# Performance work log

Hardware: AMD Instinct MI355X
Metric: run time of the kernel (lower is better)

The kernel has to match this reference:

```python
import jax, jax.numpy as jnp
import numpy as np

P = 5; G = 60; E = 256; H = 8
NPD = G // P; NP = NPD ** 3          # 1728 patch tokens
LE = 4; LD = 2; NC = 40; B = 4
MASK_RATIO = 0.75
NUM_MASK = int(MASK_RATIO * NP)      # 1296 masked, 432 visible


def setup_inputs() -> dict:
    key = jax.random.key(0)
    ki = iter(jax.random.split(key, 64))
    def n(shape, s=0.02):
        return jax.random.normal(next(ki), shape, jnp.float32) * s
    d = {
        "x": jax.random.normal(next(ki), (B, 1, G, G, G), jnp.float32),
        "noise": jax.random.uniform(next(ki), (B, NP), jnp.float32),
        "patch_w": n((E, 1, P, P, P), 0.05),
        "patch_b": jnp.zeros((E,), jnp.float32),
        "pos_embed": n((1, NP, E)),
        "dec_pos_embed": n((1, NP, E)),
        "mask_token": n((1, 1, E)),
        "pred_w": n((P ** 3, E)),
        "pred_b": jnp.zeros((P ** 3,), jnp.float32),
        "cls_w": n((NC, E)),
        "cls_b": jnp.zeros((NC,), jnp.float32),
    }
    for pre, L in (("enc", LE), ("dec", LD)):
        d[pre + "_qkv_w"] = n((L, 3 * E, E)); d[pre + "_qkv_b"] = jnp.zeros((L, 3 * E), jnp.float32)
        d[pre + "_out_w"] = n((L, E, E));     d[pre + "_out_b"] = jnp.zeros((L, E), jnp.float32)
        d[pre + "_ln1_w"] = jnp.ones((L, E), jnp.float32); d[pre + "_ln1_b"] = jnp.zeros((L, E), jnp.float32)
        d[pre + "_ln2_w"] = jnp.ones((L, E), jnp.float32); d[pre + "_ln2_b"] = jnp.zeros((L, E), jnp.float32)
        d[pre + "_ffn1_w"] = n((L, 4 * E, E)); d[pre + "_ffn1_b"] = jnp.zeros((L, 4 * E), jnp.float32)
        d[pre + "_ffn2_w"] = n((L, E, 4 * E)); d[pre + "_ffn2_b"] = jnp.zeros((L, E), jnp.float32)
    return d


def _ln(x, w, b):
    m = x.mean(-1, keepdims=True)
    v = ((x - m) ** 2).mean(-1, keepdims=True)
    return (x - m) / jnp.sqrt(v + 1e-5) * w + b


def _layer(x, qkv_w, qkv_b, out_w, out_b, l1w, l1b, l2w, l2b, f1w, f1b, f2w, f2b):
    # post-norm TransformerEncoderLayer with exact-erf GELU (dropout=0 at eval)
    Bx, S, Ex = x.shape
    dh = Ex // H
    qkv = x @ qkv_w.T + qkv_b                      # [B,S,3E]
    q, k, v = jnp.split(qkv, 3, axis=-1)
    q = q.reshape(Bx, S, H, dh); k = k.reshape(Bx, S, H, dh); v = v.reshape(Bx, S, H, dh)
    scores = jnp.einsum('bqhd,bkhd->bhqk', q, k) / np.float32(np.sqrt(dh))
    attn = jax.nn.softmax(scores, axis=-1)
    o = jnp.einsum('bhqk,bkhd->bqhd', attn, v).reshape(Bx, S, Ex)
    x = _ln(x + o @ out_w.T + out_b, l1w, l1b)
    f = jax.nn.gelu(x @ f1w.T + f1b, approximate=False) @ f2w.T + f2b
    return _ln(x + f, l2w, l2b)


def _stack(x, params, L):
    for i in range(L):
        x = _layer(x, *(a[i] for a in params))
    return x


def _forward(x, noise, patch_w, patch_b, pos_embed, dec_pos_embed, mask_token,
             enc_qkv_w, enc_qkv_b, enc_out_w, enc_out_b, enc_ln1_w, enc_ln1_b, enc_ln2_w, enc_ln2_b,
             enc_ffn1_w, enc_ffn1_b, enc_ffn2_w, enc_ffn2_b,
             dec_qkv_w, dec_qkv_b, dec_out_w, dec_out_b, dec_ln1_w, dec_ln1_b, dec_ln2_w, dec_ln2_b,
             dec_ffn1_w, dec_ffn1_b, dec_ffn2_w, dec_ffn2_b,
             pred_w, pred_b, cls_w, cls_b):
    Bx = x.shape[0]
    # patchify: [B,1,G,G,G] -> [B, NP, P^3]
    xg = x.reshape(Bx, 1, NPD, P, NPD, P, NPD, P)
    xg = xg.transpose(0, 2, 4, 6, 1, 3, 5, 7).reshape(Bx, NP, P ** 3)
    # Conv3d with stride == kernel == patch embedding over flattened patches
    tokens = xg @ patch_w.reshape(E, P ** 3).T + patch_b + pos_embed   # [B,NP,E]
    # random masking
    ids_shuffle = jnp.argsort(noise, axis=1)
    ids_mask = ids_shuffle[:, :NUM_MASK]
    ids_keep = ids_shuffle[:, NUM_MASK:]                                # [B, 432]
    mask = jnp.zeros((Bx, NP), x.dtype).at[jnp.arange(Bx)[:, None], ids_mask].set(1.0)
    x_vis = jnp.take_along_axis(tokens, ids_keep[:, :, None], axis=1)   # [B,432,E]
    enc = _stack(x_vis,
                 (enc_qkv_w, enc_qkv_b, enc_out_w, enc_out_b, enc_ln1_w, enc_ln1_b,
                  enc_ln2_w, enc_ln2_b, enc_ffn1_w, enc_ffn1_b, enc_ffn2_w, enc_ffn2_b), LE)
    cls_logits = enc.mean(axis=1) @ cls_w.T + cls_b
    # scatter encoded tokens back into full mask-token buffer (vectorized over batch)
    x_dec = jnp.broadcast_to(mask_token, (Bx, NP, E))
    x_dec = jax.vmap(lambda base, ids, e: base.at[ids].set(e))(x_dec, ids_keep, enc)
    dec = _stack(x_dec + dec_pos_embed,
                 (dec_qkv_w, dec_qkv_b, dec_out_w, dec_out_b, dec_ln1_w, dec_ln1_b,
                  dec_ln2_w, dec_ln2_b, dec_ffn1_w, dec_ffn1_b, dec_ffn2_w, dec_ffn2_b), LD)
    pred = dec @ pred_w.T + pred_b                                      # [B,NP,P^3]
    return pred, xg, mask, cls_logits


def reference(x, noise, patch_w, patch_b, pos_embed, dec_pos_embed, mask_token,
              enc_qkv_w, enc_qkv_b, enc_out_w, enc_out_b, enc_ln1_w, enc_ln1_b, enc_ln2_w, enc_ln2_b,
              enc_ffn1_w, enc_ffn1_b, enc_ffn2_w, enc_ffn2_b,
              dec_qkv_w, dec_qkv_b, dec_out_w, dec_out_b, dec_ln1_w, dec_ln1_b, dec_ln2_w, dec_ln2_b,
              dec_ffn1_w, dec_ffn1_b, dec_ffn2_w, dec_ffn2_b,
              pred_w, pred_b, cls_w, cls_b):
    return _forward(x, noise, patch_w, patch_b, pos_embed, dec_pos_embed, mask_token,
                    enc_qkv_w, enc_qkv_b, enc_out_w, enc_out_b, enc_ln1_w, enc_ln1_b, enc_ln2_w, enc_ln2_b,
                    enc_ffn1_w, enc_ffn1_b, enc_ffn2_w, enc_ffn2_b,
                    dec_qkv_w, dec_qkv_b, dec_out_w, dec_out_b, dec_ln1_w, dec_ln1_b, dec_ln2_w, dec_ln2_b,
                    dec_ffn1_w, dec_ffn1_b, dec_ffn2_w, dec_ffn2_b,
                    pred_w, pred_b, cls_w, cls_b)
```

## Files before the change

kernel.cpp:

```cpp
#include <hip/hip_runtime.h>
#include <hip/hip_bf16.h>
#include <math.h>

#define E 256
#define Hh 8
#define DH 32
#define NP 1728
#define PP3 125
#define Bb 4
#define NUM_MASKC 1296
#define NKEEP 432
#define LE 4
#define LD 2
#define NC 40

typedef __attribute__((ext_vector_type(4))) float f32x4;
typedef __attribute__((ext_vector_type(8))) short bf16x8;
typedef __attribute__((ext_vector_type(4))) short s16x4;

#define QSCALE 0.25505654708402214f

__device__ inline short f2b(float f) {
    __hip_bfloat16 h = __float2bfloat16(f);
    return *reinterpret_cast<short*>(&h);
}
__device__ inline float b2f(short s) {
    union { unsigned u; float f; } v; v.u = ((unsigned)(unsigned short)s) << 16;
    return v.f;
}
__device__ inline unsigned cvt_pk(float lo, float hi) {
    unsigned r;
    asm("v_cvt_pk_bf16_f32 %0, %1, %2" : "=v"(r) : "v"(lo), "v"(hi));
    return r;
}
__device__ inline void gl_lds16(const void* g, void* l) {
    __builtin_amdgcn_global_load_lds(
        (const __attribute__((address_space(1))) void*)g,
        (__attribute__((address_space(3))) void*)l, 16, 0, 0);
}

struct W2B { const float* src; short* dst; int n; int npad; };
struct W2BTab { W2B e[25]; };
__global__ void k_w2b(W2BTab tab) {
    W2B w = tab.e[blockIdx.y];
    int i = (blockIdx.x*256 + threadIdx.x) * 8;
    if (i + 8 <= w.n) {
        float4 a = *(const float4*)(w.src + i);
        float4 b = *(const float4*)(w.src + i + 4);
        short t[8] = {f2b(a.x),f2b(a.y),f2b(a.z),f2b(a.w),
                      f2b(b.x),f2b(b.y),f2b(b.z),f2b(b.w)};
        *(bf16x8*)(w.dst + i) = *(const bf16x8*)t;
    } else if (i < w.npad) {
        *(bf16x8*)(w.dst + i) = (bf16x8)0;
    }
}

__global__ void k_rank(const float* __restrict__ noise, int* __restrict__ shuf,
                       int* __restrict__ keep_pos, float* __restrict__ out_mask)
{
    __shared__ float ns[NP];
    int b = blockIdx.x / 7, it = blockIdx.x % 7;
    const float* nr = noise + (size_t)b*NP;
    int tid = threadIdx.x;
    for (int j = tid; j < NP; j += 256) ns[j] = nr[j];
    __syncthreads();
    int i = it*256 + tid;
    if (i < NP) {
        float ni = ns[i];
        int rank = 0;
        for (int j = 0; j < NP; ++j) {
            float nj = ns[j];
            rank += (nj < ni) || (nj == ni && j < i);
        }
        shuf[b*NP + rank] = i;
        keep_pos[b*NP + i] = (rank >= NUM_MASKC) ? (rank - NUM_MASKC) : -1;
        out_mask[b*NP + i] = (rank < NUM_MASKC) ? 1.0f : 0.0f;
    }
}

__global__ void k_xg(const float* __restrict__ x, float* __restrict__ out_xg)
{
    int bn = blockIdx.x;
    int b = bn / NP, n = bn % NP;
    int a0 = n / 144, r = n % 144, b0 = r / 12, c0 = r % 12;
    int t = threadIdx.x;
    if (t < PP3) {
        int pa = t / 25, rem = t % 25, pbq = rem / 5, pc = rem % 5;
        out_xg[(size_t)bn*PP3 + t] =
            x[(size_t)b*216000 + (size_t)(a0*5+pa)*3600 + (b0*5+pbq)*60 + (c0*5+pc)];
    }
}

__global__ void k_patch_vis(const float* __restrict__ x, const float* __restrict__ pw,
                            const float* __restrict__ pb, const float* __restrict__ pos,
                            const int* __restrict__ shuf, short* __restrict__ visb)
{
    int row = blockIdx.x;
    int b = row / NKEEP, s = row % NKEEP;
    int n = shuf[b*NP + NUM_MASKC + s];
    int a0 = n / 144, r = n % 144, b0 = r / 12, c0 = r % 12;
    __shared__ float patch[PP3];
    int t = threadIdx.x;
    if (t < PP3) {
        int pa = t / 25, rem = t % 25, pbq = rem / 5, pc = rem % 5;
        patch[t] = x[(size_t)b*216000 + (size_t)(a0*5+pa)*3600 + (b0*5+pbq)*60 + (c0*5+pc)];
    }
    __syncthreads();
    float acc = pb[t] + pos[(size_t)n*E + t];
    const float* w = pw + (size_t)t*PP3;
    for (int k = 0; k < PP3; ++k) acc += patch[k] * w[k];
    visb[(size_t)row*E + t] = f2b(acc);
}

__global__ __launch_bounds__(256) void
k_mgemm(const short* __restrict__ A, const short* __restrict__ W,
        const float* __restrict__ bias, float* __restrict__ Cf,
        short* __restrict__ Cb, int M, int N, int K, int act,
        short* __restrict__ qkvb, short* __restrict__ vTb, int S)
{
    __shared__ short As[64][64];
    __shared__ short Ws[64][64];
    int tid = threadIdx.x;
    int lane = tid & 63, wave = tid >> 6;
    int rb = blockIdx.y * 64, cb = blockIdx.x * 64;
    int wr = (wave >> 1) * 32, wc = (wave & 1) * 32;
    int fr = lane & 15, fq = lane >> 4;
    f32x4 acc[2][2];
    #pragma unroll
    for (int m = 0; m < 2; ++m)
        #pragma unroll
        for (int n = 0; n < 2; ++n) acc[m][n] = (f32x4)0.f;
    int rl = lane >> 3, cl = lane & 7;
    int r0 = 16 * wave;
    for (int kk0 = 0; kk0 < K; kk0 += 64) {
        #pragma unroll
        for (int j = 0; j < 2; ++j) {
            int r = r0 + 8*j + rl;
            int cs = cl ^ (r & 7);
            gl_lds16(A + (size_t)(rb + r)*K + kk0 + cs*8, &As[r0 + 8*j][0]);
            gl_lds16(W + (size_t)(cb + r)*K + kk0 + cs*8, &Ws[r0 + 8*j][0]);
        }
        __syncthreads();
        #pragma unroll
        for (int t = 0; t < 2; ++t) {
            int rA0 = wr + fr, rA1 = wr + 16 + fr;
            int rB0 = wc + fr, rB1 = wc + 16 + fr;
            bf16x8 a0 = *(const bf16x8*)&As[rA0][(((4*t + fq) ^ (rA0 & 7)) << 3)];
            bf16x8 a1 = *(const bf16x8*)&As[rA1][(((4*t + fq) ^ (rA1 & 7)) << 3)];
            bf16x8 b0 = *(const bf16x8*)&Ws[rB0][(((4*t + fq) ^ (rB0 & 7)) << 3)];
            bf16x8 b1 = *(const bf16x8*)&Ws[rB1][(((4*t + fq) ^ (rB1 & 7)) << 3)];
            acc[0][0] = __builtin_amdgcn_mfma_f32_16x16x32_bf16(a0, b0, acc[0][0], 0, 0, 0);
            acc[0][1] = __builtin_amdgcn_mfma_f32_16x16x32_bf16(a0, b1, acc[0][1], 0, 0, 0);
            acc[1][0] = __builtin_amdgcn_mfma_f32_16x16x32_bf16(a1, b0, acc[1][0], 0, 0, 0);
            acc[1][1] = __builtin_amdgcn_mfma_f32_16x16x32_bf16(a1, b1, acc[1][1], 0, 0, 0);
        }
        __syncthreads();
    }
    #pragma unroll
    for (int m = 0; m < 2; ++m) {
        #pragma unroll
        for (int n = 0; n < 2; ++n) {
            int col = cb + wc + n*16 + fr;
            if (col >= N) continue;
            float bv = bias[col];
            #pragma unroll
            for (int r = 0; r < 4; ++r) {
                int row = rb + wr + m*16 + fq*4 + r;
                if (row >= M) continue;
                float v = acc[m][n][r] + bv;
                if (act == 1) v = 0.5f * v * (1.f + erff(v * 0.70710678118654752f));
                if (qkvb) {
                    if (col < 512) {
                        if (col < 256) v *= QSCALE;
                        qkvb[(size_t)row*768 + col] = f2b(v);
                    } else {
                        int b = row / S, s = row - b*S;
                        int hd = col - 512;
                        vTb[((size_t)(b*Hh + (hd >> 5))*DH + (hd & 31))*S + s] = f2b(v);
                    }
                } else if (Cb) {
                    Cb[(size_t)row*N + col] = f2b(v);
                } else {
                    Cf[(size_t)row*N + col] = v;
                }
            }
        }
    }
}

__global__ __launch_bounds__(128) void
k_fattn(const short* __restrict__ qkvb, const short* __restrict__ vTb,
        short* __restrict__ o, int S)
{
    __shared__ short Ks[2][64][40];
    __shared__ short Vt[2][32][72];
    int nqt = (S + 31) >> 5;
    int bi = blockIdx.x;
    int qt = bi % nqt, bh = bi / nqt;
    int h = bh & 7, b = bh >> 3;
    int q0 = qt << 5;
    int tid = threadIdx.x;
    int lane = tid & 63, wave = tid >> 6;
    int fr = lane & 15, fq = lane >> 4;
    bf16x8 qfrag = (bf16x8)0;
    int qg = q0 + wave*16 + fr;
    if (qg < S)
        qfrag = *(const bf16x8*)(qkvb + (size_t)(b*S+qg)*768 + h*DH + 8*fq);
    f32x4 acc0 = (f32x4)0.f, acc1 = (f32x4)0.f;
    float lpart = 0.f;
    int krow = tid >> 1, kh = (tid & 1) * 16;
    int vrow = tid >> 2, vk4 = (tid & 3) * 16;
    const short* kbase = qkvb + (size_t)(b*S)*768 + 256 + h*DH + (size_t)krow*768 + kh;
    const short* vTh = vTb + (size_t)bh*DH*S + (size_t)vrow*S + vk4;
    int src1 = fr + ((fq & 1) << 5);
    int src2 = src1 + 16;
    bool sel = (fq >> 1) != 0;
    int nt = (S + 63) >> 6;
    bool tail = (S & 63) != 0;
    bf16x8 kr0, kr1, vr0, vr1;
    auto LOADF = [&](int t) {
        const short* src = kbase + (size_t)(t << 6)*768;
        kr0 = *(const bf16x8*)src;
        kr1 = *(const bf16x8*)(src + 8);
        const short* vs = vTh + (t << 6);
        vr0 = *(const bf16x8*)vs;
        vr1 = *(const bf16x8*)(vs + 8);
    };
    auto LOADT = [&](int t) {
        int kg = (t << 6) + krow;
        if (kg < S) {
            const short* src = kbase + (size_t)(t << 6)*768;
            kr0 = *(const bf16x8*)src;
            kr1 = *(const bf16x8*)(src + 8);
        } else { kr0 = (bf16x8)0; kr1 = (bf16x8)0; }
        if ((t << 6) + vk4 < S) {
            const short* vs = vTh + (t << 6);
            vr0 = *(const bf16x8*)vs;
            vr1 = *(const bf16x8*)(vs + 8);
        } else { vr0 = (bf16x8)0; vr1 = (bf16x8)0; }
    };
    auto WRITE = [&](int p) {
        *(bf16x8*)&Ks[p][krow][kh]      = kr0;
        *(bf16x8*)&Ks[p][krow][kh + 8]  = kr1;
        *(bf16x8*)&Vt[p][vrow][vk4]     = vr0;
        *(bf16x8*)&Vt[p][vrow][vk4 + 8] = vr1;
    };
    LOADF(0); WRITE(0);
    __syncthreads();
    for (int t = 0; t < nt; ++t) {
        int p = t & 1;
        bool masked = tail && (t == nt - 1);
        if (t + 1 < nt) {
            if (tail && (t + 1 == nt - 1)) LOADT(t + 1); else LOADF(t + 1);
        }
        f32x4 st[4];
        #pragma unroll
        for (int kt = 0; kt < 4; ++kt) {
            bf16x8 kf = *(const bf16x8*)&Ks[p][kt*16 + fr][8*fq];
            st[kt] = __builtin_amdgcn_mfma_f32_16x16x32_bf16(kf, qfrag, (f32x4)0.f, 0, 0, 0);
        }
        if (masked) {
            int kt0 = t << 6;
            #pragma unroll
            for (int kt = 0; kt < 4; ++kt)
                #pragma unroll
                for (int r = 0; r < 4; ++r)
                    if (kt0 + kt*16 + 4*fq + r >= S) st[kt][r] = -1e30f;
        }
        float tsum = 0.f;
        unsigned pk[4][2];
        #pragma unroll
        for (int kt = 0; kt < 4; ++kt) {
            float p0 = exp2f(st[kt][0]), p1 = exp2f(st[kt][1]);
            float p2 = exp2f(st[kt][2]), p3 = exp2f(st[kt][3]);
            tsum += (p0 + p1) + (p2 + p3);
            pk[kt][0] = cvt_pk(p0, p1);
            pk[kt][1] = cvt_pk(p2, p3);
        }
        lpart += tsum;
        #pragma unroll
        for (int t2 = 0; t2 < 2; ++t2) {
            unsigned a0 = __shfl(pk[2*t2][0], src1),   a1 = __shfl(pk[2*t2][1], src1);
            unsigned a2 = __shfl(pk[2*t2][0], src2),   a3 = __shfl(pk[2*t2][1], src2);
            unsigned b0 = __shfl(pk[2*t2+1][0], src1), b1 = __shfl(pk[2*t2+1][1], src1);
            unsigned b2 = __shfl(pk[2*t2+1][0], src2), b3 = __shfl(pk[2*t2+1][1], src2);
            union { unsigned u[4]; bf16x8 v; } B2;
            B2.u[0] = sel ? b0 : a0;
            B2.u[1] = sel ? b1 : a1;
            B2.u[2] = sel ? b2 : a2;
            B2.u[3] = sel ? b3 : a3;
            bf16x8 v0 = *(const bf16x8*)&Vt[p][fr][t2*32 + 8*fq];
            bf16x8 v1 = *(const bf16x8*)&Vt[p][16 + fr][t2*32 + 8*fq];
            acc0 = __builtin_amdgcn_mfma_f32_16x16x32_bf16(v0, B2.v, acc0, 0, 0, 0);
            acc1 = __builtin_amdgcn_mfma_f32_16x16x32_bf16(v1, B2.v, acc1, 0, 0, 0);
        }
        if (t + 1 < nt) WRITE(p ^ 1);
        __syncthreads();
    }
    float lsum = lpart;
    lsum += __shfl_xor(lsum, 16);
    lsum += __shfl_xor(lsum, 32);
    if (qg < S) {
        float inv = 1.f / lsum;
        short* op = o + (size_t)(b*S + qg)*E + h*DH;
        s16x4 o0 = { f2b(acc0[0]*inv), f2b(acc0[1]*inv), f2b(acc0[2]*inv), f2b(acc0[3]*inv) };
        s16x4 o1 = { f2b(acc1[0]*inv), f2b(acc1[1]*inv), f2b(acc1[2]*inv), f2b(acc1[3]*inv) };
        *(s16x4*)&op[4*fq]      = o0;
        *(s16x4*)&op[16 + 4*fq] = o1;
    }
}

__global__ __launch_bounds__(256) void
k_lnadd(short* __restrict__ x, const short* __restrict__ rsd,
        const float* __restrict__ w, const float* __restrict__ bv)
{
    int row = blockIdx.x*4 + (threadIdx.x >> 6);
    int lane = threadIdx.x & 63;
    int c0 = lane * 4;
    size_t base = (size_t)row*E + c0;
    s16x4 xv = *(const s16x4*)&x[base];
    s16x4 rv = *(const s16x4*)&rsd[base];
    float v[4];
    float s = 0.f, sq = 0.f;
    #pragma unroll
    for (int j = 0; j < 4; ++j) {
        v[j] = b2f(xv[j]) + b2f(rv[j]);
        s += v[j]; sq += v[j]*v[j];
    }
    #pragma unroll
    for (int off = 1; off < 64; off <<= 1) {
        s  += __shfl_xor(s, off);
        sq += __shfl_xor(sq, off);
    }
    float mean = s * (1.f/E);
    float var = fmaxf(sq * (1.f/E) - mean*mean, 0.f);
    float rstd = 1.f / sqrtf(var + 1e-5f);
    float4 wv = *(const float4*)&w[c0];
    float4 bb = *(const float4*)&bv[c0];
    s16x4 o;
    o[0] = f2b((v[0]-mean)*rstd*wv.x + bb.x);
    o[1] = f2b((v[1]-mean)*rstd*wv.y + bb.y);
    o[2] = f2b((v[2]-mean)*rstd*wv.z + bb.z);
    o[3] = f2b((v[3]-mean)*rstd*wv.w + bb.w);
    *(s16x4*)&x[base] = o;
}

__global__ void k_mean(const short* __restrict__ xv, float* __restrict__ mb)
{
    int b = blockIdx.x, tid = threadIdx.x;
    float s = 0.f;
    for (int r = 0; r < NKEEP; ++r) s += b2f(xv[((size_t)b*NKEEP + r)*E + tid]);
    mb[b*E + tid] = s * (1.f/NKEEP);
}

__global__ void k_cls(const float* __restrict__ mb, const float* __restrict__ cw,
                      const float* __restrict__ cb, float* __restrict__ out)
{
    int t = threadIdx.x;
    if (t < Bb*NC) {
        int b = t / NC, c = t % NC;
        float acc = cb[c];
        for (int k = 0; k < E; ++k) acc += mb[b*E+k]*cw[c*E+k];
        out[t] = acc;
    }
}

__global__ void k_scatter(const short* __restrict__ visb, const int* __restrict__ keep_pos,
                          const float* __restrict__ mtok, const float* __restrict__ dpos,
                          short* __restrict__ xdb)
{
    int bn = blockIdx.x; int b = bn / NP, n = bn % NP;
    int t = threadIdx.x;
    int s = keep_pos[bn];
    float base = (s >= 0) ? b2f(visb[((size_t)b*NKEEP + s)*E + t]) : mtok[t];
    xdb[(size_t)bn*E + t] = f2b(base + dpos[(size_t)n*E + t]);
}

extern "C" void kernel_launch(void* const* d_in, const int* in_sizes, int n_in,
                              void* d_out, int out_size, void* d_ws, size_t ws_size,
                              hipStream_t stream)
{
    const float* x        = (const float*)d_in[0];
    const float* noise    = (const float*)d_in[1];
    const float* patch_w  = (const float*)d_in[2];
    const float* patch_b  = (const float*)d_in[3];
    const float* pos      = (const float*)d_in[4];
    const float* dpos     = (const float*)d_in[5];
    const float* mtok     = (const float*)d_in[6];
    const float* pred_w   = (const float*)d_in[7];
    const float* pred_b   = (const float*)d_in[8];
    const float* cls_w    = (const float*)d_in[9];
    const float* cls_b    = (const float*)d_in[10];
    const float* enc_w[12]; for (int i = 0; i < 12; ++i) enc_w[i] = (const float*)d_in[11+i];
    const float* dec_w[12]; for (int i = 0; i < 12; ++i) dec_w[i] = (const float*)d_in[23+i];

    float* out = (float*)d_out;
    float* out_pred = out;
    float* out_xg   = out + 864000;
    float* out_mask = out + 1728000;
    float* out_cls  = out + 1734912;

    short* S0   = (short*)d_ws;
    short* qkvb = S0;
    short* bigb = qkvb + 5308416;
    short* vTb  = bigb + 7077888;
    short* visb = vTb  + 1769472;
    short* xdb  = visb + 442368;
    short* c1b  = xdb  + 1769472;
    short* c2b  = c1b  + 1769472;
    short* wb   = c2b  + 1769472;
    float* mb   = (float*)(wb + 4751360);
    int* shuf   = (int*)(mb + 1024);
    int* keep   = shuf + Bb*NP;

    const int LSTRIDE = 786432;
    W2BTab tab;
    int wi = 0;
    size_t off = 0;
    auto addw = [&](const float* src, int n, int npad) {
        tab.e[wi].src = src; tab.e[wi].dst = wb + off;
        tab.e[wi].n = n; tab.e[wi].npad = npad;
        ++wi; off += npad;
    };
    for (int l = 0; l < LE; ++l) {
        addw(enc_w[0] + (size_t)l*3*E*E, 3*E*E, 3*E*E);
        addw(enc_w[2] + (size_t)l*E*E,   E*E,   E*E);
        addw(enc_w[8] + (size_t)l*4*E*E, 4*E*E, 4*E*E);
        addw(enc_w[10]+ (size_t)l*4*E*E, 4*E*E, 4*E*E);
    }
    for (int l = 0; l < LD; ++l) {
        addw(dec_w[0] + (size_t)l*3*E*E, 3*E*E, 3*E*E);
        addw(dec_w[2] + (size_t)l*E*E,   E*E,   E*E);
        addw(dec_w[8] + (size_t)l*4*E*E, 4*E*E, 4*E*E);
        addw(dec_w[10]+ (size_t)l*4*E*E, 4*E*E, 4*E*E);
    }
    addw(pred_w, PP3*E, 128*E);
    hipLaunchKernelGGL(k_w2b, dim3(128, 25), dim3(256), 0, stream, tab);

    auto gemm = [&](const short* A, const short* W, const float* bias,
                    float* Cf, short* Cb, int M, int N, int K, int act,
                    short* qb, short* vb, int Sv) {
        dim3 g((N+63)/64, (M+63)/64);
        hipLaunchKernelGGL(k_mgemm, g, dim3(256), 0, stream, A, W, bias,
                           Cf, Cb, M, N, K, act, qb, vb, Sv);
    };

    auto layer = [&](short* xbuf, int Bl, int S, const float* const* Wp,
                     const short* wbase, int l) {
        int M = Bl * S;
        int nqt = (S + 31) / 32;
        const short* wq = wbase + (size_t)l*LSTRIDE;
        const short* wo = wq + 3*E*E;
        const short* w1 = wo + E*E;
        const short* w2 = w1 + 4*E*E;
        gemm(xbuf, wq, Wp[1] + l*3*E, nullptr, nullptr, M, 3*E, E, 0, qkvb, vTb, S);
        k_fattn<<<Bl*Hh*nqt, 128, 0, stream>>>(qkvb, vTb, c1b, S);
        gemm(c1b, wo, Wp[3] + l*E, nullptr, c2b, M, E, E, 0, nullptr, nullptr, 1);
        k_lnadd<<<M/4, 256, 0, stream>>>(xbuf, c2b, Wp[4] + l*E, Wp[5] + l*E);
        gemm(xbuf, w1, Wp[9] + l*4*E, nullptr, bigb, M, 4*E, E, 1, nullptr, nullptr, 1);
        gemm(bigb, w2, Wp[11] + l*E, nullptr, c2b, M, E, 4*E, 0, nullptr, nullptr, 1);
        k_lnadd<<<M/4, 256, 0, stream>>>(xbuf, c2b, Wp[6] + l*E, Wp[7] + l*E);
    };

    k_rank<<<Bb*7, 256, 0, stream>>>(noise, shuf, keep, out_mask);
    k_xg<<<Bb*NP, 128, 0, stream>>>(x, out_xg);
    k_patch_vis<<<Bb*NKEEP, 256, 0, stream>>>(x, patch_w, patch_b, pos, shuf, visb);

    const short* enc_wb = wb;
    const short* dec_wb = wb + (size_t)LE*LSTRIDE;
    const short* pred_wb = wb + (size_t)(LE+LD)*LSTRIDE;

    for (int l = 0; l < LE; ++l) layer(visb, Bb, NKEEP, enc_w, enc_wb, l);

    k_mean<<<Bb, 256, 0, stream>>>(visb, mb);
    k_cls<<<1, 256, 0, stream>>>(mb, cls_w, cls_b, out_cls);

    k_scatter<<<Bb*NP, 256, 0, stream>>>(visb, keep, mtok, dpos, xdb);
    for (int l = 0; l < LD; ++l) layer(xdb, Bb, NP, dec_w, dec_wb, l);
    gemm(xdb, pred_wb, pred_b, out_pred, nullptr, Bb*NP, PP3, E, 0, nullptr, nullptr, 1);
}
```

Before: 555.2 us.

## Double-buffer GEMM LDS tiles and widen attention blocks to 64 queries

The GEMM kernel now double-buffers its shared-memory A/W tiles, issuing the next k-tile's global-to-LDS loads before computing on the current one. This is meant to overlap memory latency with MFMA work. The attention kernel goes from 128 to 256 threads, 4 waves covering 64 queries per block, and each thread now loads one 8-element K and V chunk. This halves the number of blocks and spreads K/V tile loading across more threads per block. The GEMM loop keeps only one barrier per iteration, and the hidden part of the loop must still order the buffer swap correctly. Doubling LDS and fewer attention blocks may lower occupancy or parallelism for the small token counts.

```diff
diff --git a/kernel.cpp b/kernel.cpp
--- a/kernel.cpp
+++ b/kernel.cpp
@@ -118,8 +118,8 @@
         short* __restrict__ Cb, int M, int N, int K, int act,
         short* __restrict__ qkvb, short* __restrict__ vTb, int S)
 {
-    __shared__ short As[64][64];
-    __shared__ short Ws[64][64];
+    __shared__ short As[2][64][64];
+    __shared__ short Ws[2][64][64];
     int tid = threadIdx.x;
     int lane = tid & 63, wave = tid >> 6;
     int rb = blockIdx.y * 64, cb = blockIdx.x * 64;
@@ -132,23 +132,30 @@
         for (int n = 0; n < 2; ++n) acc[m][n] = (f32x4)0.f;
     int rl = lane >> 3, cl = lane & 7;
     int r0 = 16 * wave;
-    for (int kk0 = 0; kk0 < K; kk0 += 64) {
+    int nk = K >> 6;
+    auto stage = [&](int p, int t) {
+        int kk0 = t << 6;
         #pragma unroll
         for (int j = 0; j < 2; ++j) {
             int r = r0 + 8*j + rl;
             int cs = cl ^ (r & 7);
-            gl_lds16(A + (size_t)(rb + r)*K + kk0 + cs*8, &As[r0 + 8*j][0]);
-            gl_lds16(W + (size_t)(cb + r)*K + kk0 + cs*8, &Ws[r0 + 8*j][0]);
-        }
-        __syncthreads();
-        #pragma unroll
-        for (int t = 0; t < 2; ++t) {
+            gl_lds16(A + (size_t)(rb + r)*K + kk0 + cs*8, &As[p][r0 + 8*j][0]);
+            gl_lds16(W + (size_t)(cb + r)*K + kk0 + cs*8, &Ws[p][r0 + 8*j][0]);
+        }
+    };
+    stage(0, 0);
+    __syncthreads();
+    for (int t = 0; t < nk; ++t) {
+        int p = t & 1;
+        if (t + 1 < nk) stage(p ^ 1, t + 1);
+        #pragma unroll
+        for (int tt = 0; tt < 2; ++tt) {
             int rA0 = wr + fr, rA1 = wr + 16 + fr;
             int rB0 = wc + fr, rB1 = wc + 16 + fr;
-            bf16x8 a0 = *(const bf16x8*)&As[rA0][(((4*t + fq) ^ (rA0 & 7)) << 3)];
-            bf16x8 a1 = *(const bf16x8*)&As[rA1][(((4*t + fq) ^ (rA1 & 7)) << 3)];
-            bf16x8 b0 = *(const bf16x8*)&Ws[rB0][(((4*t + fq) ^ (rB0 & 7)) << 3)];
-            bf16x8 b1 = *(const bf16x8*)&Ws[rB1][(((4*t + fq) ^ (rB1 & 7)) << 3)];
+            bf16x8 a0 = *(const bf16x8*)&As[p][rA0][(((4*tt + fq) ^ (rA0 & 7)) << 3)];
+            bf16x8 a1 = *(const bf16x8*)&As[p][rA1][(((4*tt + fq) ^ (rA1 & 7)) << 3)];
+            bf16x8 b0 = *(const bf16x8*)&Ws[p][rB0][(((4*tt + fq) ^ (rB0 & 7)) << 3)];
+            bf16x8 b1 = *(const bf16x8*)&Ws[p][rB1][(((4*tt + fq) ^ (rB1 & 7)) << 3)];
             acc[0][0] = __builtin_amdgcn_mfma_f32_16x16x32_bf16(a0, b0, acc[0][0], 0, 0, 0);
             acc[0][1] = __builtin_amdgcn_mfma_f32_16x16x32_bf16(a0, b1, acc[0][1], 0, 0, 0);
             acc[1][0] = __builtin_amdgcn_mfma_f32_16x16x32_bf16(a1, b0, acc[1][0], 0, 0, 0);
@@ -188,17 +195,17 @@
     }
 }
 
-__global__ __launch_bounds__(128) void
+__global__ __launch_bounds__(256) void
 k_fattn(const short* __restrict__ qkvb, const short* __restrict__ vTb,
         short* __restrict__ o, int S)
 {
     __shared__ short Ks[2][64][40];
     __shared__ short Vt[2][32][72];
-    int nqt = (S + 31) >> 5;
+    int nqt = (S + 63) >> 6;
     int bi = blockIdx.x;
     int qt = bi % nqt, bh = bi / nqt;
     int h = bh & 7, b = bh >> 3;
-    int q0 = qt << 5;
+    int q0 = qt << 6;
     int tid = threadIdx.x;
     int lane = tid & 63, wave = tid >> 6;
     int fr = lane & 15, fq = lane >> 4;
@@ -208,44 +215,34 @@
         qfrag = *(const bf16x8*)(qkvb + (size_t)(b*S+qg)*768 + h*DH + 8*fq);
     f32x4 acc0 = (f32x4)0.f, acc1 = (f32x4)0.f;
     float lpart = 0.f;
-    int krow = tid >> 1, kh = (tid & 1) * 16;
-    int vrow = tid >> 2, vk4 = (tid & 3) * 16;
+    int krow = tid >> 2, kh = (tid & 3) * 8;
+    int vrow = tid >> 3, vk = (tid & 7) * 8;
     const short* kbase = qkvb + (size_t)(b*S)*768 + 256 + h*DH + (size_t)krow*768 + kh;
-    const short* vTh = vTb + (size_t)bh*DH*S + (size_t)vrow*S + vk4;
+    const short* vTh = vTb + (size_t)bh*DH*S + (size_t)vrow*S + vk;
     int src1 = fr + ((fq & 1) << 5);
     int src2 = src1 + 16;
     bool sel = (fq >> 1) != 0;
     int nt = (S + 63) >> 6;
     bool tail = (S & 63) != 0;
-    bf16x8 kr0, kr1, vr0, vr1;
+    bf16x8 kr0, vr0;
     auto LOADF = [&](int t) {
-        const short* src = kbase + (size_t)(t << 6)*768;
-        kr0 = *(const bf16x8*)src;
-        kr1 = *(const bf16x8*)(src + 8);
-        const short* vs = vTh + (t << 6);
-        vr0 = *(const bf16x8*)vs;
-        vr1 = *(const bf16x8*)(vs + 8);
+        kr0 = *(const bf16x8*)(kbase + (size_t)(t << 6)*768);
+        vr0 = *(const bf16x8*)(vTh + (t << 6));
     };
     auto LOADT = [&](int t) {
-        int kg = (t << 6) + krow;
-        if (kg < S) {
-            const short* src = kbase + (size_t)(t << 6)*768;
-            kr0 = *(const bf16x8*)src;
-            kr1 = *(const bf16x8*)(src + 8);
-        } else { kr0 = (bf16x8)0; kr1 = (bf16x8)0; }
-        if ((t << 6) + vk4 < S) {
-            const short* vs = vTh + (t << 6);
-            vr0 = *(const bf16x8*)vs;
-            vr1 = *(const bf16x8*)(vs + 8);
-        } else { vr0 = (bf16x8)0; vr1 = (bf16x8)0; }
+        if ((t << 6) + krow < S)
+            kr0 = *(const bf16x8*)(kbase + (size_t)(t << 6)*768);
+        else kr0 = (bf16x8)0;
+        if ((t << 6) + vk < S)
+            vr0 = *(const bf16x8*)(vTh + (t << 6));
+        else vr0 = (bf16x8)0;
     };
     auto WRITE = [&](int p) {
-        *(bf16x8*)&Ks[p][krow][kh]      = kr0;
-        *(bf16x8*)&Ks[p][krow][kh + 8]  = kr1;
-        *(bf16x8*)&Vt[p][vrow][vk4]     = vr0;
-        *(bf16x8*)&Vt[p][vrow][vk4 + 8] = vr1;
-    };
-    LOADF(0); WRITE(0);
+        *(bf16x8*)&Ks[p][krow][kh] = kr0;
+        *(bf16x8*)&Vt[p][vrow][vk] = vr0;
+    };
+    if (tail && nt == 1) LOADT(0); else LOADF(0);
+    WRITE(0);
     __syncthreads();
     for (int t = 0; t < nt; ++t) {
         int p = t & 1;
@@ -448,13 +445,13 @@
     auto layer = [&](short* xbuf, int Bl, int S, const float* const* Wp,
                      const short* wbase, int l) {
         int M = Bl * S;
-        int nqt = (S + 31) / 32;
+        int nqt = (S + 63) / 64;
         const short* wq = wbase + (size_t)l*LSTRIDE;
         const short* wo = wq + 3*E*E;
         const short* w1 = wo + E*E;
         const short* w2 = w1 + 4*E*E;
         gemm(xbuf, wq, Wp[1] + l*3*E, nullptr, nullptr, M, 3*E, E, 0, qkvb, vTb, S);
-        k_fattn<<<Bl*Hh*nqt, 128, 0, stream>>>(qkvb, vTb, c1b, S);
+        k_fattn<<<Bl*Hh*nqt, 256, 0, stream>>>(qkvb, vTb, c1b, S);
         gemm(c1b, wo, Wp[3] + l*E, nullptr, c2b, M, E, E, 0, nullptr, nullptr, 1);
         k_lnadd<<<M/4, 256, 0, stream>>>(xbuf, c2b, Wp[4] + l*E, Wp[5] + l*E);
         gemm(xbuf, w1, Wp[9] + l*4*E, nullptr, bigb, M, 4*E, E, 1, nullptr, nullptr, 1);
```

New measurement: 573.7 us. 1.03x slower.

## Fuse output and FFN2 projections with residual add and LayerNorm

Applied to the files above, without the earlier changes.

Adds a k_gemm_ln kernel that computes a full 256-wide output row block per workgroup, then adds bias and residual and applies LayerNorm in the epilogue, using cross-wave reductions through LDS. This replaces the separate N=256 GEMMs plus k_lnadd launches, removing the bf16 intermediate round trip and one launch per LayerNorm. It also fixes tail-tile loading in attention when there is only one key tile. The trade-off is a smaller grid (M/64 blocks), which lowers parallelism for the 1728-row encoder shapes, and it assumes M is a multiple of 64.

```diff
diff --git a/kernel.cpp b/kernel.cpp
--- a/kernel.cpp
+++ b/kernel.cpp
@@ -183,6 +183,110 @@
                 } else {
                     Cf[(size_t)row*N + col] = v;
                 }
+            }
+        }
+    }
+}
+
+__global__ __launch_bounds__(256) void
+k_gemm_ln(const short* __restrict__ A, const short* __restrict__ W,
+          const float* __restrict__ bias, short* __restrict__ xres,
+          const float* __restrict__ lnw, const float* __restrict__ lnb,
+          int M, int K)
+{
+    __shared__ short As[64][64];
+    __shared__ short Ws[256][64];
+    __shared__ float rsum[4][64];
+    __shared__ float rsq[4][64];
+    int tid = threadIdx.x;
+    int lane = tid & 63, wave = tid >> 6;
+    int rb = blockIdx.x * 64;
+    int fr = lane & 15, fq = lane >> 4;
+    f32x4 acc[4][4];
+    #pragma unroll
+    for (int mi = 0; mi < 4; ++mi)
+        #pragma unroll
+        for (int nj = 0; nj < 4; ++nj) acc[mi][nj] = (f32x4)0.f;
+    int rl = lane >> 3, cl = lane & 7;
+    for (int kk0 = 0; kk0 < K; kk0 += 64) {
+        #pragma unroll
+        for (int j = 0; j < 2; ++j) {
+            int r = wave*16 + 8*j + rl;
+            int cs = cl ^ (r & 7);
+            gl_lds16(A + (size_t)(rb + r)*K + kk0 + cs*8, &As[wave*16 + 8*j][0]);
+        }
+        #pragma unroll
+        for (int j = 0; j < 8; ++j) {
+            int r = wave*64 + 8*j + rl;
+            int cs = cl ^ (r & 7);
+            gl_lds16(W + (size_t)r*K + kk0 + cs*8, &Ws[wave*64 + 8*j][0]);
+        }
+        __syncthreads();
+        #pragma unroll
+        for (int t = 0; t < 2; ++t) {
+            bf16x8 av[4], bv[4];
+            #pragma unroll
+            for (int mi = 0; mi < 4; ++mi) {
+                int rA = mi*16 + fr;
+                av[mi] = *(const bf16x8*)&As[rA][(((4*t + fq) ^ (rA & 7)) << 3)];
+            }
+            #pragma unroll
+            for (int nj = 0; nj < 4; ++nj) {
+                int rB = wave*64 + nj*16 + fr;
+                bv[nj] = *(const bf16x8*)&Ws[rB][(((4*t + fq) ^ (rB & 7)) << 3)];
+            }
+            #pragma unroll
+            for (int mi = 0; mi < 4; ++mi)
+                #pragma unroll
+                for (int nj = 0; nj < 4; ++nj)
+                    acc[mi][nj] = __builtin_amdgcn_mfma_f32_16x16x32_bf16(
+                        av[mi], bv[nj], acc[mi][nj], 0, 0, 0);
+        }
+        __syncthreads();
+    }
+    float lw[4], lb[4], bs[4];
+    #pragma unroll
+    for (int nj = 0; nj < 4; ++nj) {
+        int col = wave*64 + nj*16 + fr;
+        bs[nj] = bias[col]; lw[nj] = lnw[col]; lb[nj] = lnb[col];
+    }
+    #pragma unroll
+    for (int mi = 0; mi < 4; ++mi) {
+        #pragma unroll
+        for (int r = 0; r < 4; ++r) {
+            int rowl = mi*16 + fq*4 + r;
+            size_t rowg = (size_t)(rb + rowl);
+            float s = 0.f, q = 0.f;
+            #pragma unroll
+            for (int nj = 0; nj < 4; ++nj) {
+                int col = wave*64 + nj*16 + fr;
+                float v = acc[mi][nj][r] + bs[nj] + b2f(xres[rowg*E + col]);
+                acc[mi][nj][r] = v;
+                s += v; q += v*v;
+            }
+            s += __shfl_xor(s, 1); q += __shfl_xor(q, 1);
+            s += __shfl_xor(s, 2); q += __shfl_xor(q, 2);
+            s += __shfl_xor(s, 4); q += __shfl_xor(q, 4);
+            s += __shfl_xor(s, 8); q += __shfl_xor(q, 8);
+            if (fr == 0) { rsum[wave][rowl] = s; rsq[wave][rowl] = q; }
+        }
+    }
+    __syncthreads();
+    #pragma unroll
+    for (int mi = 0; mi < 4; ++mi) {
+        #pragma unroll
+        for (int r = 0; r < 4; ++r) {
+            int rowl = mi*16 + fq*4 + r;
+            size_t rowg = (size_t)(rb + rowl);
+            float tot  = rsum[0][rowl] + rsum[1][rowl] + rsum[2][rowl] + rsum[3][rowl];
+            float totq = rsq[0][rowl]  + rsq[1][rowl]  + rsq[2][rowl]  + rsq[3][rowl];
+            float mean = tot * (1.f/E);
+            float var  = fmaxf(totq * (1.f/E) - mean*mean, 0.f);
+            float rstd = 1.f / sqrtf(var + 1e-5f);
+            #pragma unroll
+            for (int nj = 0; nj < 4; ++nj) {
+                int col = wave*64 + nj*16 + fr;
+                xres[rowg*E + col] = f2b((acc[mi][nj][r] - mean)*rstd*lw[nj] + lb[nj]);
             }
         }
     }
@@ -245,7 +349,8 @@
         *(bf16x8*)&Vt[p][vrow][vk4]     = vr0;
         *(bf16x8*)&Vt[p][vrow][vk4 + 8] = vr1;
     };
-    LOADF(0); WRITE(0);
+    if (tail && nt == 1) LOADT(0); else LOADF(0);
+    WRITE(0);
     __syncthreads();
     for (int t = 0; t < nt; ++t) {
         int p = t & 1;
@@ -310,41 +415,6 @@
     }
 }
 
-__global__ __launch_bounds__(256) void
-k_lnadd(short* __restrict__ x, const short* __restrict__ rsd,
-        const float* __restrict__ w, const float* __restrict__ bv)
-{
-    int row = blockIdx.x*4 + (threadIdx.x >> 6);
-    int lane = threadIdx.x & 63;
-    int c0 = lane * 4;
-    size_t base = (size_t)row*E + c0;
-    s16x4 xv = *(const s16x4*)&x[base];
-    s16x4 rv = *(const s16x4*)&rsd[base];
-    float v[4];
-    float s = 0.f, sq = 0.f;
-    #pragma unroll
-    for (int j = 0; j < 4; ++j) {
-        v[j] = b2f(xv[j]) + b2f(rv[j]);
-        s += v[j]; sq += v[j]*v[j];
-    }
-    #pragma unroll
-    for (int off = 1; off < 64; off <<= 1) {
-        s  += __shfl_xor(s, off);
-        sq += __shfl_xor(sq, off);
-    }
-    float mean = s * (1.f/E);
-    float var = fmaxf(sq * (1.f/E) - mean*mean, 0.f);
-    float rstd = 1.f / sqrtf(var + 1e-5f);
-    float4 wv = *(const float4*)&w[c0];
-    float4 bb = *(const float4*)&bv[c0];
-    s16x4 o;
-    o[0] = f2b((v[0]-mean)*rstd*wv.x + bb.x);
-    o[1] = f2b((v[1]-mean)*rstd*wv.y + bb.y);
-    o[2] = f2b((v[2]-mean)*rstd*wv.z + bb.z);
-    o[3] = f2b((v[3]-mean)*rstd*wv.w + bb.w);
-    *(s16x4*)&x[base] = o;
-}
-
 __global__ void k_mean(const short* __restrict__ xv, float* __restrict__ mb)
 {
     int b = blockIdx.x, tid = threadIdx.x;
@@ -455,11 +525,11 @@
         const short* w2 = w1 + 4*E*E;
         gemm(xbuf, wq, Wp[1] + l*3*E, nullptr, nullptr, M, 3*E, E, 0, qkvb, vTb, S);
         k_fattn<<<Bl*Hh*nqt, 128, 0, stream>>>(qkvb, vTb, c1b, S);
-        gemm(c1b, wo, Wp[3] + l*E, nullptr, c2b, M, E, E, 0, nullptr, nullptr, 1);
-        k_lnadd<<<M/4, 256, 0, stream>>>(xbuf, c2b, Wp[4] + l*E, Wp[5] + l*E);
+        k_gemm_ln<<<M/64, 256, 0, stream>>>(c1b, wo, Wp[3] + l*E, xbuf,
+                                            Wp[4] + l*E, Wp[5] + l*E, M, E);
         gemm(xbuf, w1, Wp[9] + l*4*E, nullptr, bigb, M, 4*E, E, 1, nullptr, nullptr, 1);
-        gemm(bigb, w2, Wp[11] + l*E, nullptr, c2b, M, E, 4*E, 0, nullptr, nullptr, 1);
-        k_lnadd<<<M/4, 256, 0, stream>>>(xbuf, c2b, Wp[6] + l*E, Wp[7] + l*E);
+        k_gemm_ln<<<M/64, 256, 0, stream>>>(bigb, w2, Wp[11] + l*E, xbuf,
+                                            Wp[6] + l*E, Wp[7] + l*E, M, 4*E);
     };
 
     k_rank<<<Bb*7, 256, 0, stream>>>(noise, shuf, keep, out_mask);
```

Measured after the change: 656.9 us. +18.3%, slower.

## Double-buffer GEMM tiles with register prefetch instead of direct global-to-LDS loads

Applied to the files above, without the earlier changes.

The bf16 GEMM kernel now stages the A and W tiles through registers into two LDS buffers. The next K tile is loaded from global memory while MFMAs run on the current one, and the old direct global_load_lds path with a barrier per tile is removed. This is meant to hide global load latency behind compute, at the cost of double the LDS use and more registers. The attention kernel also gains a fix so the first tile uses the tail-masked loader when there is only one tile.

```diff
diff --git a/kernel.cpp b/kernel.cpp
--- a/kernel.cpp
+++ b/kernel.cpp
@@ -32,11 +32,6 @@
     unsigned r;
     asm("v_cvt_pk_bf16_f32 %0, %1, %2" : "=v"(r) : "v"(lo), "v"(hi));
     return r;
-}
-__device__ inline void gl_lds16(const void* g, void* l) {
-    __builtin_amdgcn_global_load_lds(
-        (const __attribute__((address_space(1))) void*)g,
-        (__attribute__((address_space(3))) void*)l, 16, 0, 0);
 }
 
 struct W2B { const float* src; short* dst; int n; int npad; };
@@ -118,8 +113,8 @@
         short* __restrict__ Cb, int M, int N, int K, int act,
         short* __restrict__ qkvb, short* __restrict__ vTb, int S)
 {
-    __shared__ short As[64][64];
-    __shared__ short Ws[64][64];
+    __shared__ short As[2][64][64];
+    __shared__ short Ws[2][64][64];
     int tid = threadIdx.x;
     int lane = tid & 63, wave = tid >> 6;
     int rb = blockIdx.y * 64, cb = blockIdx.x * 64;
@@ -130,30 +125,47 @@
     for (int m = 0; m < 2; ++m)
         #pragma unroll
         for (int n = 0; n < 2; ++n) acc[m][n] = (f32x4)0.f;
-    int rl = lane >> 3, cl = lane & 7;
-    int r0 = 16 * wave;
-    for (int kk0 = 0; kk0 < K; kk0 += 64) {
-        #pragma unroll
-        for (int j = 0; j < 2; ++j) {
-            int r = r0 + 8*j + rl;
-            int cs = cl ^ (r & 7);
-            gl_lds16(A + (size_t)(rb + r)*K + kk0 + cs*8, &As[r0 + 8*j][0]);
-            gl_lds16(W + (size_t)(cb + r)*K + kk0 + cs*8, &Ws[r0 + 8*j][0]);
-        }
-        __syncthreads();
-        #pragma unroll
-        for (int t = 0; t < 2; ++t) {
+    int sr = tid >> 2;
+    int sc0 = (tid & 3) * 2;
+    const short* Arow = A + (size_t)(rb + sr)*K + sc0*8;
+    const short* Wrow = W + (size_t)(cb + sr)*K + sc0*8;
+    int c0x = (sc0     ^ (sr & 7)) * 8;
+    int c1x = ((sc0+1) ^ (sr & 7)) * 8;
+    bf16x8 ra0, ra1, rw0, rw1;
+    auto LOADR = [&](int t) {
+        const short* a = Arow + (t << 6);
+        ra0 = *(const bf16x8*)a;
+        ra1 = *(const bf16x8*)(a + 8);
+        const short* w = Wrow + (t << 6);
+        rw0 = *(const bf16x8*)w;
+        rw1 = *(const bf16x8*)(w + 8);
+    };
+    auto WRITE = [&](int p) {
+        *(bf16x8*)&As[p][sr][c0x] = ra0;
+        *(bf16x8*)&As[p][sr][c1x] = ra1;
+        *(bf16x8*)&Ws[p][sr][c0x] = rw0;
+        *(bf16x8*)&Ws[p][sr][c1x] = rw1;
+    };
+    int nk = K >> 6;
+    LOADR(0); WRITE(0);
+    __syncthreads();
+    for (int t = 0; t < nk; ++t) {
+        int p = t & 1;
+        if (t + 1 < nk) LOADR(t + 1);
+        #pragma unroll
+        for (int tt = 0; tt < 2; ++tt) {
             int rA0 = wr + fr, rA1 = wr + 16 + fr;
             int rB0 = wc + fr, rB1 = wc + 16 + fr;
-            bf16x8 a0 = *(const bf16x8*)&As[rA0][(((4*t + fq) ^ (rA0 & 7)) << 3)];
-            bf16x8 a1 = *(const bf16x8*)&As[rA1][(((4*t + fq) ^ (rA1 & 7)) << 3)];
-            bf16x8 b0 = *(const bf16x8*)&Ws[rB0][(((4*t + fq) ^ (rB0 & 7)) << 3)];
-            bf16x8 b1 = *(const bf16x8*)&Ws[rB1][(((4*t + fq) ^ (rB1 & 7)) << 3)];
+            bf16x8 a0 = *(const bf16x8*)&As[p][rA0][(((4*tt + fq) ^ (rA0 & 7)) << 3)];
+            bf16x8 a1 = *(const bf16x8*)&As[p][rA1][(((4*tt + fq) ^ (rA1 & 7)) << 3)];
+            bf16x8 b0 = *(const bf16x8*)&Ws[p][rB0][(((4*tt + fq) ^ (rB0 & 7)) << 3)];
+            bf16x8 b1 = *(const bf16x8*)&Ws[p][rB1][(((4*tt + fq) ^ (rB1 & 7)) << 3)];
             acc[0][0] = __builtin_amdgcn_mfma_f32_16x16x32_bf16(a0, b0, acc[0][0], 0, 0, 0);
             acc[0][1] = __builtin_amdgcn_mfma_f32_16x16x32_bf16(a0, b1, acc[0][1], 0, 0, 0);
             acc[1][0] = __builtin_amdgcn_mfma_f32_16x16x32_bf16(a1, b0, acc[1][0], 0, 0, 0);
             acc[1][1] = __builtin_amdgcn_mfma_f32_16x16x32_bf16(a1, b1, acc[1][1], 0, 0, 0);
         }
+        if (t + 1 < nk) WRITE(p ^ 1);
         __syncthreads();
     }
     #pragma unroll
@@ -245,7 +257,8 @@
         *(bf16x8*)&Vt[p][vrow][vk4]     = vr0;
         *(bf16x8*)&Vt[p][vrow][vk4 + 8] = vr1;
     };
-    LOADF(0); WRITE(0);
+    if (tail && nt == 1) LOADT(0); else LOADF(0);
+    WRITE(0);
     __syncthreads();
     for (int t = 0; t < nt; ++t) {
         int p = t & 1;
```

Measured after the change: 558.1 us. About the same (+0.5%).
